# Performance work log

Hardware: AMD Instinct MI355X
Metric: run time of the kernel (lower is better)

Reference implementation:

```python
import jax, jax.numpy as jnp
import numpy as np

EMBED_DIM = 1024
N_HEAD = 16
HEAD_DIM = EMBED_DIM // N_HEAD


def setup_inputs() -> dict:
    key = jax.random.key(0)
    ks = jax.random.split(key, 6)
    B, T, C = 2, 2048, EMBED_DIM
    s = 1.0 / np.sqrt(C)
    return {
        "x": jax.random.normal(ks[0], (B, T, C), dtype=jnp.float32),
        "Wq": jax.random.normal(ks[1], (C, C), dtype=jnp.float32) * s,
        "Wk": jax.random.normal(ks[2], (C, C), dtype=jnp.float32) * s,
        "Wv": jax.random.normal(ks[3], (C, C), dtype=jnp.float32) * s,
        "Wo": jax.random.normal(ks[4], (C, C), dtype=jnp.float32) * s,
        "bo": jax.random.normal(ks[5], (C,), dtype=jnp.float32) * 0.01,
    }


def reference(x, Wq, Wk, Wv, Wo, bo):
    B, T, C = x.shape
    H, D = N_HEAD, HEAD_DIM
    # projections: torch nn.Linear computes x @ W.T; weights here stored as (out,in)
    q = (x @ Wq.T).reshape(B, T, H, D).transpose(0, 2, 1, 3)  # [B,H,T,D]
    k = (x @ Wk.T).reshape(B, T, H, D).transpose(0, 2, 1, 3)
    v = (x @ Wv.T).reshape(B, T, H, D).transpose(0, 2, 1, 3)
    energy = jnp.einsum("bhqd,bhkd->bhqk", q, k)
    causal = jnp.tril(jnp.ones((T, T), dtype=bool))
    energy = jnp.where(causal[None, None], energy, -jnp.inf)
    # NOTE: original scales by 1/sqrt(embed_dim), not 1/sqrt(head_dim)
    attn = jax.nn.softmax(energy * (1.0 / jnp.sqrt(jnp.float32(C))), axis=-1)
    out = jnp.einsum("bhqk,bhkd->bhqd", attn, v)
    out = out.transpose(0, 2, 1, 3).reshape(B, T, C)
    return out @ Wo.T + bo
```

## Files before the change

kernel.cpp:

```cpp
#include <hip/hip_runtime.h>
#include <hip/hip_bf16.h>
#include <stdint.h>


typedef __bf16 bf16_t;
typedef __bf16 bf16x8 __attribute__((ext_vector_type(8)));
typedef float f32x4 __attribute__((ext_vector_type(4)));
typedef unsigned short u16x8 __attribute__((ext_vector_type(8)));
typedef unsigned short u16x4 __attribute__((ext_vector_type(4)));

#define MFMA(a, b, c) __builtin_amdgcn_mfma_f32_16x16x32_bf16((a), (b), (c), 0, 0, 0)

__device__ __forceinline__ void gload_lds16(const void* g, void* l) {
  __builtin_amdgcn_global_load_lds(
      (const __attribute__((address_space(1))) void*)g,
      (__attribute__((address_space(3))) void*)l, 16, 0, 0);
}

__global__ __launch_bounds__(256) void cvt_f32_to_bf16(const float* __restrict__ in,
                                                       bf16_t* __restrict__ out, int n) {
  int i = (blockIdx.x * 256 + threadIdx.x) * 8;
  if (i + 8 > n) return;
  const float4 a = *reinterpret_cast<const float4*>(in + i);
  const float4 b = *reinterpret_cast<const float4*>(in + i + 4);
  bf16x8 o;
  o[0] = (bf16_t)a.x; o[1] = (bf16_t)a.y; o[2] = (bf16_t)a.z; o[3] = (bf16_t)a.w;
  o[4] = (bf16_t)b.x; o[5] = (bf16_t)b.y; o[6] = (bf16_t)b.z; o[7] = (bf16_t)b.w;
  *reinterpret_cast<bf16x8*>(out + i) = o;
}

__global__ __launch_bounds__(256) void cvt4_f32_to_bf16(
    const float* __restrict__ i0, const float* __restrict__ i1,
    const float* __restrict__ i2, const float* __restrict__ i3,
    bf16_t* __restrict__ o0, bf16_t* __restrict__ o1,
    bf16_t* __restrict__ o2, bf16_t* __restrict__ o3) {
  const float* in; bf16_t* out;
  switch (blockIdx.y) {
    case 0: in = i0; out = o0; break;
    case 1: in = i1; out = o1; break;
    case 2: in = i2; out = o2; break;
    default: in = i3; out = o3; break;
  }
  int i = (blockIdx.x * 256 + threadIdx.x) * 8;
  const float4 a = *reinterpret_cast<const float4*>(in + i);
  const float4 b = *reinterpret_cast<const float4*>(in + i + 4);
  bf16x8 o;
  o[0] = (bf16_t)a.x; o[1] = (bf16_t)a.y; o[2] = (bf16_t)a.z; o[3] = (bf16_t)a.w;
  o[4] = (bf16_t)b.x; o[5] = (bf16_t)b.y; o[6] = (bf16_t)b.z; o[7] = (bf16_t)b.w;
  *reinterpret_cast<bf16x8*>(out + i) = o;
}

__global__ __launch_bounds__(256, 2) void qkv_gemm(
    const bf16_t* __restrict__ X, const bf16_t* __restrict__ Wq,
    const bf16_t* __restrict__ Wk, const bf16_t* __restrict__ Wv,
    bf16_t* __restrict__ Q, bf16_t* __restrict__ Ko, bf16_t* __restrict__ Vt) {
  constexpr int Kdim = 1024;
  const int z = blockIdx.z;
  const bf16_t* __restrict__ W = (z == 0) ? Wq : (z == 1) ? Wk : Wv;

  __shared__ __align__(16) bf16_t As[128][64];
  __shared__ __align__(16) bf16_t Bs[128][64];

  const int tid = threadIdx.x;
  const int lane = tid & 63;
  const int w = tid >> 6;
  const int wr = w >> 1, wc = w & 1;
  const int ln = lane & 15, lh = lane >> 4;
  const int brow = blockIdx.y * 128;
  const int bcol = blockIdx.x * 128;

  const int soff = (w * 4) * 1024 + lane * 16;

  f32x4 acc[4][4] = {};

  for (int k0 = 0; k0 < Kdim; k0 += 64) {
#pragma unroll
    for (int s = 0; s < 4; ++s) {
      const int off = soff + s * 1024;
      const int row = off >> 7, colb = off & 127;
      gload_lds16((const char*)X + ((size_t)(brow + row) * Kdim + k0) * 2 + colb,
                  (char*)&As[0][0] + (w * 4 + s) * 1024);
      gload_lds16((const char*)W + ((size_t)(bcol + row) * Kdim + k0) * 2 + colb,
                  (char*)&Bs[0][0] + (w * 4 + s) * 1024);
    }
    __syncthreads();
#pragma unroll
    for (int kk = 0; kk < 2; ++kk) {
      bf16x8 af[4], bfm[4];
#pragma unroll
      for (int i = 0; i < 4; ++i)
        af[i] = *reinterpret_cast<const bf16x8*>(&As[wr * 64 + i * 16 + ln][kk * 32 + lh * 8]);
#pragma unroll
      for (int j = 0; j < 4; ++j)
        bfm[j] = *reinterpret_cast<const bf16x8*>(&Bs[wc * 64 + j * 16 + ln][kk * 32 + lh * 8]);
#pragma unroll
      for (int i = 0; i < 4; ++i)
#pragma unroll
        for (int j = 0; j < 4; ++j)
          acc[i][j] = MFMA(af[i], bfm[j], acc[i][j]);
    }
    __syncthreads();
  }

#pragma unroll
  for (int i = 0; i < 4; ++i) {
    const int m0 = brow + wr * 64 + i * 16 + lh * 4;
    const int b = m0 >> 11;
    const int t0 = m0 & 2047;
#pragma unroll
    for (int j = 0; j < 4; ++j) {
      const int n = bcol + wc * 64 + j * 16 + ln;
      const int h = n >> 6, d = n & 63;
      if (z == 2) {
        u16x4 pk;
#pragma unroll
        for (int r = 0; r < 4; ++r)
          pk[r] = __builtin_bit_cast(unsigned short, (bf16_t)acc[i][j][r]);
        *reinterpret_cast<u16x4*>(&Vt[(size_t)((b * 16 + h) * 64 + d) * 2048 + t0]) = pk;
      } else {
        bf16_t* __restrict__ dst = (z == 0) ? Q : Ko;
        const float sc = (z == 0) ? 0.03125f : 1.0f;
#pragma unroll
        for (int r = 0; r < 4; ++r)
          dst[(size_t)((b * 16 + h) * 2048 + t0 + r) * 64 + d] = (bf16_t)(acc[i][j][r] * sc);
      }
    }
  }
}

#define SWZK(r, c) ((c) ^ (((r) & 7) << 3))
#define SWZP(r, c) ((c) ^ ((((r) >> 2) & 3) << 4))
__global__ __launch_bounds__(256, 4) void attn_fwd(
    const bf16_t* __restrict__ q,
    const bf16_t* __restrict__ kmat,
    const bf16_t* __restrict__ vt,
    bf16_t* __restrict__ o)
{
  const int bh = blockIdx.x;
  const int h = bh & 15, b = bh >> 4;
  const int qblk = blockIdx.y;
  const int tid = threadIdx.x, w = tid >> 6, lane = tid & 63;
  const int ln = lane & 15, lh = lane >> 4;

  __shared__ __align__(16) bf16_t Ks[64][64];
  __shared__ __align__(16) bf16_t Vts[64][64];
  __shared__ __align__(16) bf16_t Ps[4][16][64];

  const size_t base = (size_t)bh * 2048 * 64;
  const int q0 = qblk * 64 + w * 16;

  bf16x8 qf[2];
#pragma unroll
  for (int kk = 0; kk < 2; ++kk)
    qf[kk] = *reinterpret_cast<const bf16x8*>(
        &q[base + (size_t)(q0 + ln) * 64 + kk * 32 + lh * 8]);

  f32x4 o_acc[4] = {};
  float m_s[4], l_s[4];
#pragma unroll
  for (int r = 0; r < 4; ++r) { m_s[r] = -1e30f; l_s[r] = 0.0f; }

  const int ck0 = w * 4;

  const int ntiles = qblk + 1;
  for (int kt = 0; kt < ntiles; ++kt) {
    const int k0 = kt * 64;
    __syncthreads();
#pragma unroll
    for (int s = 0; s < 4; ++s) {
      const int c = ck0 + s;
      const int off = (c & 7) * 1024 + lane * 16;
      const int row = off >> 7;
      const int colb = (off & 127) ^ ((row & 7) << 4);
      if (c < 8)
        gload_lds16((const char*)kmat + (base + (size_t)(k0 + row) * 64) * 2 + colb,
                    (char*)&Ks[0][0] + (c & 7) * 1024);
      else
        gload_lds16((const char*)vt + (base + (size_t)row * 2048 + k0) * 2 + colb,
                    (char*)&Vts[0][0] + (c & 7) * 1024);
    }
    __syncthreads();

    f32x4 sfr[4] = {};
#pragma unroll
    for (int kk = 0; kk < 2; ++kk) {
      bf16x8 kf[4];
#pragma unroll
      for (int j = 0; j < 4; ++j) {
        const int kr = j * 16 + ln;
        kf[j] = *reinterpret_cast<const bf16x8*>(&Ks[kr][SWZK(kr, kk * 32 + lh * 8)]);
      }
#pragma unroll
      for (int j = 0; j < 4; ++j)
        sfr[j] = MFMA(qf[kk], kf[j], sfr[j]);
    }

    float alpha[4];
#pragma unroll
    for (int r = 0; r < 4; ++r) {
      const int qg = q0 + lh * 4 + r;
      float mx = -1e30f;
#pragma unroll
      for (int j = 0; j < 4; ++j) {
        const int key = k0 + j * 16 + ln;
        float sv = (key <= qg) ? sfr[j][r] : -1e30f;
        sfr[j][r] = sv;
        mx = fmaxf(mx, sv);
      }
#pragma unroll
      for (int off = 1; off < 16; off <<= 1) mx = fmaxf(mx, __shfl_xor(mx, off));
      const float mnew = fmaxf(m_s[r], mx);
      const float a = __expf(m_s[r] - mnew);
      m_s[r] = mnew;
      float rs = 0.0f;
#pragma unroll
      for (int j = 0; j < 4; ++j) {
        const float p = __expf(sfr[j][r] - mnew);
        sfr[j][r] = p;
        rs += p;
      }
#pragma unroll
      for (int off = 1; off < 16; off <<= 1) rs += __shfl_xor(rs, off);
      l_s[r] = l_s[r] * a + rs;
      alpha[r] = a;
    }

#pragma unroll
    for (int j = 0; j < 4; ++j)
#pragma unroll
      for (int r = 0; r < 4; ++r) {
        const int pr = lh * 4 + r;
        Ps[w][pr][SWZP(pr, j * 16 + ln)] = (bf16_t)sfr[j][r];
      }
    asm volatile("s_waitcnt lgkmcnt(0)" ::: "memory");

#pragma unroll
    for (int j = 0; j < 4; ++j)
#pragma unroll
      for (int r = 0; r < 4; ++r) o_acc[j][r] *= alpha[r];

#pragma unroll
    for (int kk = 0; kk < 2; ++kk) {
      bf16x8 pa, vf[4];
      pa = *reinterpret_cast<const bf16x8*>(&Ps[w][ln][SWZP(ln, kk * 32 + lh * 8)]);
#pragma unroll
      for (int j = 0; j < 4; ++j) {
        const int vr = j * 16 + ln;
        vf[j] = *reinterpret_cast<const bf16x8*>(&Vts[vr][SWZK(vr, kk * 32 + lh * 8)]);
      }
#pragma unroll
      for (int j = 0; j < 4; ++j)
        o_acc[j] = MFMA(pa, vf[j], o_acc[j]);
    }
  }

#pragma unroll
  for (int r = 0; r < 4; ++r) {
    const float inv = 1.0f / l_s[r];
    const int t = q0 + lh * 4 + r;
#pragma unroll
    for (int j = 0; j < 4; ++j) {
      const int d = j * 16 + ln;
      o[(size_t)(b * 2048 + t) * 1024 + h * 64 + d] = (bf16_t)(o_acc[j][r] * inv);
    }
  }
}

__global__ __launch_bounds__(256, 2) void out_gemm(
    const bf16_t* __restrict__ X, const bf16_t* __restrict__ W,
    const float* __restrict__ bias, float* __restrict__ Y) {
  constexpr int Kdim = 1024;
  __shared__ __align__(16) bf16_t As[128][64];
  __shared__ __align__(16) bf16_t Bs[128][64];

  const int tid = threadIdx.x;
  const int lane = tid & 63;
  const int w = tid >> 6;
  const int wr = w >> 1, wc = w & 1;
  const int ln = lane & 15, lh = lane >> 4;
  const int brow = blockIdx.y * 128;
  const int bcol = blockIdx.x * 128;
  const int soff = (w * 4) * 1024 + lane * 16;

  f32x4 acc[4][4] = {};

  for (int k0 = 0; k0 < Kdim; k0 += 64) {
#pragma unroll
    for (int s = 0; s < 4; ++s) {
      const int off = soff + s * 1024;
      const int row = off >> 7, colb = off & 127;
      gload_lds16((const char*)X + ((size_t)(brow + row) * Kdim + k0) * 2 + colb,
                  (char*)&As[0][0] + (w * 4 + s) * 1024);
      gload_lds16((const char*)W + ((size_t)(bcol + row) * Kdim + k0) * 2 + colb,
                  (char*)&Bs[0][0] + (w * 4 + s) * 1024);
    }
    __syncthreads();
#pragma unroll
    for (int kk = 0; kk < 2; ++kk) {
      bf16x8 af[4], bfm[4];
#pragma unroll
      for (int i = 0; i < 4; ++i)
        af[i] = *reinterpret_cast<const bf16x8*>(&As[wr * 64 + i * 16 + ln][kk * 32 + lh * 8]);
#pragma unroll
      for (int j = 0; j < 4; ++j)
        bfm[j] = *reinterpret_cast<const bf16x8*>(&Bs[wc * 64 + j * 16 + ln][kk * 32 + lh * 8]);
#pragma unroll
      for (int i = 0; i < 4; ++i)
#pragma unroll
        for (int j = 0; j < 4; ++j)
          acc[i][j] = MFMA(af[i], bfm[j], acc[i][j]);
    }
    __syncthreads();
  }

#pragma unroll
  for (int i = 0; i < 4; ++i) {
    const int m0 = brow + wr * 64 + i * 16 + lh * 4;
#pragma unroll
    for (int j = 0; j < 4; ++j) {
      const int n = bcol + wc * 64 + j * 16 + ln;
      const float bv = bias[n];
#pragma unroll
      for (int r = 0; r < 4; ++r)
        Y[(size_t)(m0 + r) * 1024 + n] = acc[i][j][r] + bv;
    }
  }
}

extern "C" void kernel_launch(void* const* d_in, const int* in_sizes, int n_in,
                              void* d_out, int out_size, void* d_ws, size_t ws_size,
                              hipStream_t stream) {
  const float* x  = (const float*)d_in[0];
  const float* Wq = (const float*)d_in[1];
  const float* Wk = (const float*)d_in[2];
  const float* Wv = (const float*)d_in[3];
  const float* Wo = (const float*)d_in[4];
  const float* bo = (const float*)d_in[5];

  char* ws = (char*)d_ws;
  bf16_t* xb  = (bf16_t*)(ws);
  bf16_t* wqb = (bf16_t*)(ws + (size_t)(8u  << 20));
  bf16_t* wkb = (bf16_t*)(ws + (size_t)(10u << 20));
  bf16_t* wvb = (bf16_t*)(ws + (size_t)(12u << 20));
  bf16_t* wob = (bf16_t*)(ws + (size_t)(14u << 20));
  bf16_t* qb  = (bf16_t*)(ws + (size_t)(16u << 20));
  bf16_t* kb  = (bf16_t*)(ws + (size_t)(24u << 20));
  bf16_t* vtb = (bf16_t*)(ws + (size_t)(32u << 20));
  bf16_t* ob  = (bf16_t*)(ws + (size_t)(40u << 20));

  cvt_f32_to_bf16<<<2048, 256, 0, stream>>>(x, xb, 4096 * 1024);
  cvt4_f32_to_bf16<<<dim3(512, 4), 256, 0, stream>>>(Wq, Wk, Wv, Wo, wqb, wkb, wvb, wob);

  qkv_gemm<<<dim3(8, 32, 3), 256, 0, stream>>>(xb, wqb, wkb, wvb, qb, kb, vtb);
  attn_fwd<<<dim3(32, 32), 256, 0, stream>>>(qb, kb, vtb, ob);
  out_gemm<<<dim3(8, 32), 256, 0, stream>>>(ob, wob, bo, (float*)d_out);
}
```

Baseline: 227.3 us.

## Load K/V fragments directly from global, drop LDS staging and block syncs in attention

The attention kernel stops staging K and V^T tiles in shared memory with two __syncthreads per tile. Each wave now loads its K and V fragments straight from global memory into registers, relying on cache for reuse across the four waves. The change also remaps blockIdx.y so heavy and light causal q-blocks are interleaved, and it applies the causal mask only on the diagonal tile. The cost is more global/L2 traffic per wave, since each wave reloads the same K/V, plus higher register pressure from holding V fragments for the whole tile.

```diff
diff --git a/kernel.cpp b/kernel.cpp
--- a/kernel.cpp
+++ b/kernel.cpp
@@ -128,7 +128,6 @@
   }
 }
 
-#define SWZK(r, c) ((c) ^ (((r) & 7) << 3))
 #define SWZP(r, c) ((c) ^ ((((r) >> 2) & 3) << 4))
 __global__ __launch_bounds__(256, 4) void attn_fwd(
     const bf16_t* __restrict__ q,
@@ -138,15 +137,16 @@
 {
   const int bh = blockIdx.x;
   const int h = bh & 15, b = bh >> 4;
-  const int qblk = blockIdx.y;
+  const int y = blockIdx.y;
+  const int qblk = (y < 16) ? y : 47 - y;
   const int tid = threadIdx.x, w = tid >> 6, lane = tid & 63;
   const int ln = lane & 15, lh = lane >> 4;
 
-  __shared__ __align__(16) bf16_t Ks[64][64];
-  __shared__ __align__(16) bf16_t Vts[64][64];
   __shared__ __align__(16) bf16_t Ps[4][16][64];
 
   const size_t base = (size_t)bh * 2048 * 64;
+  const bf16_t* __restrict__ kb = kmat + base;
+  const bf16_t* __restrict__ vb = vt + base;
   const int q0 = qblk * 64 + w * 16;
 
   bf16x8 qf[2];
@@ -160,69 +160,81 @@
 #pragma unroll
   for (int r = 0; r < 4; ++r) { m_s[r] = -1e30f; l_s[r] = 0.0f; }
 
-  const int ck0 = w * 4;
-
-  const int ntiles = qblk + 1;
-  for (int kt = 0; kt < ntiles; ++kt) {
+  for (int kt = 0; kt <= qblk; ++kt) {
     const int k0 = kt * 64;
-    __syncthreads();
-#pragma unroll
-    for (int s = 0; s < 4; ++s) {
-      const int c = ck0 + s;
-      const int off = (c & 7) * 1024 + lane * 16;
-      const int row = off >> 7;
-      const int colb = (off & 127) ^ ((row & 7) << 4);
-      if (c < 8)
-        gload_lds16((const char*)kmat + (base + (size_t)(k0 + row) * 64) * 2 + colb,
-                    (char*)&Ks[0][0] + (c & 7) * 1024);
-      else
-        gload_lds16((const char*)vt + (base + (size_t)row * 2048 + k0) * 2 + colb,
-                    (char*)&Vts[0][0] + (c & 7) * 1024);
-    }
-    __syncthreads();
+
+    bf16x8 vf[2][4];
+#pragma unroll
+    for (int kk = 0; kk < 2; ++kk)
+#pragma unroll
+      for (int j = 0; j < 4; ++j)
+        vf[kk][j] = *reinterpret_cast<const bf16x8*>(
+            &vb[(size_t)(j * 16 + ln) * 2048 + k0 + kk * 32 + lh * 8]);
 
     f32x4 sfr[4] = {};
 #pragma unroll
     for (int kk = 0; kk < 2; ++kk) {
       bf16x8 kf[4];
 #pragma unroll
-      for (int j = 0; j < 4; ++j) {
-        const int kr = j * 16 + ln;
-        kf[j] = *reinterpret_cast<const bf16x8*>(&Ks[kr][SWZK(kr, kk * 32 + lh * 8)]);
+      for (int j = 0; j < 4; ++j)
+        kf[j] = *reinterpret_cast<const bf16x8*>(
+            &kb[(size_t)(k0 + j * 16 + ln) * 64 + kk * 32 + lh * 8]);
+#pragma unroll
+      for (int j = 0; j < 4; ++j)
+        sfr[j] = MFMA(qf[kk], kf[j], sfr[j]);
+    }
+
+    float alpha[4];
+    if (kt == qblk) {
+#pragma unroll
+      for (int r = 0; r < 4; ++r) {
+        const int qg = q0 + lh * 4 + r;
+        float mx = -1e30f;
+#pragma unroll
+        for (int j = 0; j < 4; ++j) {
+          const int key = k0 + j * 16 + ln;
+          float sv = (key <= qg) ? sfr[j][r] : -1e30f;
+          sfr[j][r] = sv;
+          mx = fmaxf(mx, sv);
+        }
+#pragma unroll
+        for (int off = 1; off < 16; off <<= 1) mx = fmaxf(mx, __shfl_xor(mx, off));
+        const float mnew = fmaxf(m_s[r], mx);
+        const float a = __expf(m_s[r] - mnew);
+        m_s[r] = mnew;
+        float rs = 0.0f;
+#pragma unroll
+        for (int j = 0; j < 4; ++j) {
+          const float p = __expf(sfr[j][r] - mnew);
+          sfr[j][r] = p;
+          rs += p;
+        }
+#pragma unroll
+        for (int off = 1; off < 16; off <<= 1) rs += __shfl_xor(rs, off);
+        l_s[r] = l_s[r] * a + rs;
+        alpha[r] = a;
       }
-#pragma unroll
-      for (int j = 0; j < 4; ++j)
-        sfr[j] = MFMA(qf[kk], kf[j], sfr[j]);
-    }
-
-    float alpha[4];
-#pragma unroll
-    for (int r = 0; r < 4; ++r) {
-      const int qg = q0 + lh * 4 + r;
-      float mx = -1e30f;
-#pragma unroll
-      for (int j = 0; j < 4; ++j) {
-        const int key = k0 + j * 16 + ln;
-        float sv = (key <= qg) ? sfr[j][r] : -1e30f;
-        sfr[j][r] = sv;
-        mx = fmaxf(mx, sv);
+    } else {
+#pragma unroll
+      for (int r = 0; r < 4; ++r) {
+        float mx = fmaxf(fmaxf(sfr[0][r], sfr[1][r]), fmaxf(sfr[2][r], sfr[3][r]));
+#pragma unroll
+        for (int off = 1; off < 16; off <<= 1) mx = fmaxf(mx, __shfl_xor(mx, off));
+        const float mnew = fmaxf(m_s[r], mx);
+        const float a = __expf(m_s[r] - mnew);
+        m_s[r] = mnew;
+        float rs = 0.0f;
+#pragma unroll
+        for (int j = 0; j < 4; ++j) {
+          const float p = __expf(sfr[j][r] - mnew);
+          sfr[j][r] = p;
+          rs += p;
+        }
+#pragma unroll
+        for (int off = 1; off < 16; off <<= 1) rs += __shfl_xor(rs, off);
+        l_s[r] = l_s[r] * a + rs;
+        alpha[r] = a;
       }
-#pragma unroll
-      for (int off = 1; off < 16; off <<= 1) mx = fmaxf(mx, __shfl_xor(mx, off));
-      const float mnew = fmaxf(m_s[r], mx);
-      const float a = __expf(m_s[r] - mnew);
-      m_s[r] = mnew;
-      float rs = 0.0f;
-#pragma unroll
-      for (int j = 0; j < 4; ++j) {
-        const float p = __expf(sfr[j][r] - mnew);
-        sfr[j][r] = p;
-        rs += p;
-      }
-#pragma unroll
-      for (int off = 1; off < 16; off <<= 1) rs += __shfl_xor(rs, off);
-      l_s[r] = l_s[r] * a + rs;
-      alpha[r] = a;
     }
 
 #pragma unroll
@@ -241,16 +253,10 @@
 
 #pragma unroll
     for (int kk = 0; kk < 2; ++kk) {
-      bf16x8 pa, vf[4];
-      pa = *reinterpret_cast<const bf16x8*>(&Ps[w][ln][SWZP(ln, kk * 32 + lh * 8)]);
-#pragma unroll
-      for (int j = 0; j < 4; ++j) {
-        const int vr = j * 16 + ln;
-        vf[j] = *reinterpret_cast<const bf16x8*>(&Vts[vr][SWZK(vr, kk * 32 + lh * 8)]);
-      }
-#pragma unroll
-      for (int j = 0; j < 4; ++j)
-        o_acc[j] = MFMA(pa, vf[j], o_acc[j]);
+      bf16x8 pa = *reinterpret_cast<const bf16x8*>(&Ps[w][ln][SWZP(ln, kk * 32 + lh * 8)]);
+#pragma unroll
+      for (int j = 0; j < 4; ++j)
+        o_acc[j] = MFMA(pa, vf[kk][j], o_acc[j]);
     }
   }
 
```

New measurement: 268.0 us. 1.18x slower.

## Balance causal attention work by pairing short and long query blocks per workgroup

Applied to the files above, without the earlier changes.

The attention kernel now uses 128-thread blocks that each handle two 32-row query blocks, one from the start and one from the end of the sequence, so every block does roughly equal causal work. Wave 0 loads the K tile and wave 1 loads the V tile. Causal masking is skipped for key tiles that lie entirely below the diagonal. The cost is fewer waves per block to hide latency, and each K/V tile load is shared across only 32 query rows instead of 64, which doubles K/V traffic.

```diff
diff --git a/kernel.cpp b/kernel.cpp
--- a/kernel.cpp
+++ b/kernel.cpp
@@ -130,7 +130,7 @@
 
 #define SWZK(r, c) ((c) ^ (((r) & 7) << 3))
 #define SWZP(r, c) ((c) ^ ((((r) >> 2) & 3) << 4))
-__global__ __launch_bounds__(256, 4) void attn_fwd(
+__global__ __launch_bounds__(128, 4) void attn_fwd(
     const bf16_t* __restrict__ q,
     const bf16_t* __restrict__ kmat,
     const bf16_t* __restrict__ vt,
@@ -138,130 +138,139 @@
 {
   const int bh = blockIdx.x;
   const int h = bh & 15, b = bh >> 4;
-  const int qblk = blockIdx.y;
+  const int y = blockIdx.y;
   const int tid = threadIdx.x, w = tid >> 6, lane = tid & 63;
   const int ln = lane & 15, lh = lane >> 4;
 
   __shared__ __align__(16) bf16_t Ks[64][64];
   __shared__ __align__(16) bf16_t Vts[64][64];
-  __shared__ __align__(16) bf16_t Ps[4][16][64];
+  __shared__ __align__(16) bf16_t Ps[2][16][64];
 
   const size_t base = (size_t)bh * 2048 * 64;
-  const int q0 = qblk * 64 + w * 16;
-
-  bf16x8 qf[2];
-#pragma unroll
-  for (int kk = 0; kk < 2; ++kk)
-    qf[kk] = *reinterpret_cast<const bf16x8*>(
-        &q[base + (size_t)(q0 + ln) * 64 + kk * 32 + lh * 8]);
-
-  f32x4 o_acc[4] = {};
-  float m_s[4], l_s[4];
-#pragma unroll
-  for (int r = 0; r < 4; ++r) { m_s[r] = -1e30f; l_s[r] = 0.0f; }
-
-  const int ck0 = w * 4;
-
-  const int ntiles = qblk + 1;
-  for (int kt = 0; kt < ntiles; ++kt) {
-    const int k0 = kt * 64;
-    __syncthreads();
-#pragma unroll
-    for (int s = 0; s < 4; ++s) {
-      const int c = ck0 + s;
-      const int off = (c & 7) * 1024 + lane * 16;
-      const int row = off >> 7;
-      const int colb = (off & 127) ^ ((row & 7) << 4);
-      if (c < 8)
-        gload_lds16((const char*)kmat + (base + (size_t)(k0 + row) * 64) * 2 + colb,
-                    (char*)&Ks[0][0] + (c & 7) * 1024);
-      else
-        gload_lds16((const char*)vt + (base + (size_t)row * 2048 + k0) * 2 + colb,
-                    (char*)&Vts[0][0] + (c & 7) * 1024);
-    }
-    __syncthreads();
-
-    f32x4 sfr[4] = {};
-#pragma unroll
-    for (int kk = 0; kk < 2; ++kk) {
-      bf16x8 kf[4];
+  const bf16_t* __restrict__ kb = kmat + base;
+  const bf16_t* __restrict__ vb = vt + base;
+
+  for (int seg = 0; seg < 2; ++seg) {
+    const int qq = seg ? (63 - y) : y;
+    const int q0 = qq * 32 + w * 16;
+
+    bf16x8 qf[2];
+#pragma unroll
+    for (int kk = 0; kk < 2; ++kk)
+      qf[kk] = *reinterpret_cast<const bf16x8*>(
+          &q[base + (size_t)(q0 + ln) * 64 + kk * 32 + lh * 8]);
+
+    f32x4 o_acc[4] = {};
+    float m_s[4], l_s[4];
+#pragma unroll
+    for (int r = 0; r < 4; ++r) { m_s[r] = -1e30f; l_s[r] = 0.0f; }
+
+    const int ntiles = (qq >> 1) + 1;
+    for (int kt = 0; kt < ntiles; ++kt) {
+      const int k0 = kt * 64;
+      __syncthreads();
+#pragma unroll
+      for (int s = 0; s < 8; ++s) {
+        const int off = s * 1024 + lane * 16;
+        const int row = off >> 7;
+        const int colb = (off & 127) ^ ((row & 7) << 4);
+        if (w == 0)
+          gload_lds16((const char*)kb + ((size_t)(k0 + row) * 64) * 2 + colb,
+                      (char*)&Ks[0][0] + s * 1024);
+        else
+          gload_lds16((const char*)vb + ((size_t)row * 2048 + k0) * 2 + colb,
+                      (char*)&Vts[0][0] + s * 1024);
+      }
+      __syncthreads();
+
+      f32x4 sfr[4] = {};
+#pragma unroll
+      for (int kk = 0; kk < 2; ++kk) {
+        bf16x8 kf[4];
+#pragma unroll
+        for (int j = 0; j < 4; ++j) {
+          const int kr = j * 16 + ln;
+          kf[j] = *reinterpret_cast<const bf16x8*>(&Ks[kr][SWZK(kr, kk * 32 + lh * 8)]);
+        }
+#pragma unroll
+        for (int j = 0; j < 4; ++j)
+          sfr[j] = MFMA(qf[kk], kf[j], sfr[j]);
+      }
+
+      const bool diag = (k0 + 63 > q0);
+      float alpha[4];
+#pragma unroll
+      for (int r = 0; r < 4; ++r) {
+        const int qg = q0 + lh * 4 + r;
+        float mx;
+        if (diag) {
+          mx = -1e30f;
+#pragma unroll
+          for (int j = 0; j < 4; ++j) {
+            const int key = k0 + j * 16 + ln;
+            float sv = (key <= qg) ? sfr[j][r] : -1e30f;
+            sfr[j][r] = sv;
+            mx = fmaxf(mx, sv);
+          }
+        } else {
+          mx = fmaxf(fmaxf(sfr[0][r], sfr[1][r]), fmaxf(sfr[2][r], sfr[3][r]));
+        }
+#pragma unroll
+        for (int off = 1; off < 16; off <<= 1) mx = fmaxf(mx, __shfl_xor(mx, off));
+        const float mnew = fmaxf(m_s[r], mx);
+        const float a = __expf(m_s[r] - mnew);
+        m_s[r] = mnew;
+        float rs = 0.0f;
+#pragma unroll
+        for (int j = 0; j < 4; ++j) {
+          const float p = __expf(sfr[j][r] - mnew);
+          sfr[j][r] = p;
+          rs += p;
+        }
+#pragma unroll
+        for (int off = 1; off < 16; off <<= 1) rs += __shfl_xor(rs, off);
+        l_s[r] = l_s[r] * a + rs;
+        alpha[r] = a;
+      }
+
+#pragma unroll
+      for (int j = 0; j < 4; ++j)
+#pragma unroll
+        for (int r = 0; r < 4; ++r) {
+          const int pr = lh * 4 + r;
+          Ps[w][pr][SWZP(pr, j * 16 + ln)] = (bf16_t)sfr[j][r];
+        }
+      asm volatile("s_waitcnt lgkmcnt(0)" ::: "memory");
+
+#pragma unroll
+      for (int j = 0; j < 4; ++j)
+#pragma unroll
+        for (int r = 0; r < 4; ++r) o_acc[j][r] *= alpha[r];
+
+#pragma unroll
+      for (int kk = 0; kk < 2; ++kk) {
+        bf16x8 pa = *reinterpret_cast<const bf16x8*>(&Ps[w][ln][SWZP(ln, kk * 32 + lh * 8)]);
+        bf16x8 vf[4];
+#pragma unroll
+        for (int j = 0; j < 4; ++j) {
+          const int vr = j * 16 + ln;
+          vf[j] = *reinterpret_cast<const bf16x8*>(&Vts[vr][SWZK(vr, kk * 32 + lh * 8)]);
+        }
+#pragma unroll
+        for (int j = 0; j < 4; ++j)
+          o_acc[j] = MFMA(pa, vf[j], o_acc[j]);
+      }
+    }
+
+#pragma unroll
+    for (int r = 0; r < 4; ++r) {
+      const float inv = 1.0f / l_s[r];
+      const int t = q0 + lh * 4 + r;
 #pragma unroll
       for (int j = 0; j < 4; ++j) {
-        const int kr = j * 16 + ln;
-        kf[j] = *reinterpret_cast<const bf16x8*>(&Ks[kr][SWZK(kr, kk * 32 + lh * 8)]);
-      }
-#pragma unroll
-      for (int j = 0; j < 4; ++j)
-        sfr[j] = MFMA(qf[kk], kf[j], sfr[j]);
-    }
-
-    float alpha[4];
-#pragma unroll
-    for (int r = 0; r < 4; ++r) {
-      const int qg = q0 + lh * 4 + r;
-      float mx = -1e30f;
-#pragma unroll
-      for (int j = 0; j < 4; ++j) {
-        const int key = k0 + j * 16 + ln;
-        float sv = (key <= qg) ? sfr[j][r] : -1e30f;
-        sfr[j][r] = sv;
-        mx = fmaxf(mx, sv);
-      }
-#pragma unroll
-      for (int off = 1; off < 16; off <<= 1) mx = fmaxf(mx, __shfl_xor(mx, off));
-      const float mnew = fmaxf(m_s[r], mx);
-      const float a = __expf(m_s[r] - mnew);
-      m_s[r] = mnew;
-      float rs = 0.0f;
-#pragma unroll
-      for (int j = 0; j < 4; ++j) {
-        const float p = __expf(sfr[j][r] - mnew);
-        sfr[j][r] = p;
-        rs += p;
-      }
-#pragma unroll
-      for (int off = 1; off < 16; off <<= 1) rs += __shfl_xor(rs, off);
-      l_s[r] = l_s[r] * a + rs;
-      alpha[r] = a;
-    }
-
-#pragma unroll
-    for (int j = 0; j < 4; ++j)
-#pragma unroll
-      for (int r = 0; r < 4; ++r) {
-        const int pr = lh * 4 + r;
-        Ps[w][pr][SWZP(pr, j * 16 + ln)] = (bf16_t)sfr[j][r];
-      }
-    asm volatile("s_waitcnt lgkmcnt(0)" ::: "memory");
-
-#pragma unroll
-    for (int j = 0; j < 4; ++j)
-#pragma unroll
-      for (int r = 0; r < 4; ++r) o_acc[j][r] *= alpha[r];
-
-#pragma unroll
-    for (int kk = 0; kk < 2; ++kk) {
-      bf16x8 pa, vf[4];
-      pa = *reinterpret_cast<const bf16x8*>(&Ps[w][ln][SWZP(ln, kk * 32 + lh * 8)]);
-#pragma unroll
-      for (int j = 0; j < 4; ++j) {
-        const int vr = j * 16 + ln;
-        vf[j] = *reinterpret_cast<const bf16x8*>(&Vts[vr][SWZK(vr, kk * 32 + lh * 8)]);
-      }
-#pragma unroll
-      for (int j = 0; j < 4; ++j)
-        o_acc[j] = MFMA(pa, vf[j], o_acc[j]);
-    }
-  }
-
-#pragma unroll
-  for (int r = 0; r < 4; ++r) {
-    const float inv = 1.0f / l_s[r];
-    const int t = q0 + lh * 4 + r;
-#pragma unroll
-    for (int j = 0; j < 4; ++j) {
-      const int d = j * 16 + ln;
-      o[(size_t)(b * 2048 + t) * 1024 + h * 64 + d] = (bf16_t)(o_acc[j][r] * inv);
+        const int d = j * 16 + ln;
+        o[(size_t)(b * 2048 + t) * 1024 + h * 64 + d] = (bf16_t)(o_acc[j][r] * inv);
+      }
     }
   }
 }
@@ -352,6 +361,6 @@
   cvt4_f32_to_bf16<<<dim3(512, 4), 256, 0, stream>>>(Wq, Wk, Wv, Wo, wqb, wkb, wvb, wob);
 
   qkv_gemm<<<dim3(8, 32, 3), 256, 0, stream>>>(xb, wqb, wkb, wvb, qb, kb, vtb);
-  attn_fwd<<<dim3(32, 32), 256, 0, stream>>>(qb, kb, vtb, ob);
+  attn_fwd<<<dim3(32, 32), 128, 0, stream>>>(qb, kb, vtb, ob);
   out_gemm<<<dim3(8, 32), 256, 0, stream>>>(ob, wob, bo, (float*)d_out);
 }
```

Result: no change. 226.8 us (-0.2%).
